# Optimization experiments

Hardware: AMD Instinct MI355X
Metric: run time of the kernel (lower is better)

Reference implementation:

```python
import jax, jax.numpy as jnp
import numpy as np

KERNEL = (7, 7)
NUM_CH = 4
EPS = 1e-06
ROPE_BASE = 10000.0


def _rel_dist():
    coords = [np.arange(k, dtype=np.float32) - k // 2 for k in KERNEL]
    g = np.meshgrid(*coords, indexing='ij')
    d = np.sqrt(sum(gi ** 2 for gi in g))
    return jnp.asarray(d.reshape(-1)), float(d.max())


def silu(x):
    return x * jax.nn.sigmoid(x)


def rmsnorm(x, w):
    rms = jnp.sqrt(jnp.mean(x * x, axis=-1, keepdims=True) + EPS)
    return x / rms * w


def apply_rope(x):
    # x: (B, L, H, D); positions run over dim -2 (matches torch default)
    H, D = x.shape[-2], x.shape[-1]
    half = D // 2
    pos = jnp.arange(H, dtype=jnp.float32)
    freqs = 1.0 / (ROPE_BASE ** (jnp.arange(half, dtype=x.dtype) / half))
    ang = pos[:, None] * freqs  # (H, half)
    cos, sin = jnp.cos(ang), jnp.sin(ang)
    x1, x2 = x[..., :half], x[..., half:2 * half]
    return jnp.concatenate([x1 * cos - x2 * sin, x1 * sin + x2 * cos], axis=-1)


def unfold2d(x):
    # x: (B, Hs, Ws, C) -> (B, Hs, Ws, k1*k2, C), row-major kernel order
    B, Hs, Ws, C = x.shape
    k1, k2 = KERNEL
    xp = jnp.pad(x, ((0, 0), ((k1 - 1) // 2, k1 // 2), ((k2 - 1) // 2, k2 // 2), (0, 0)))
    wins = [xp[:, i:i + Hs, j:j + Ws, :] for i in range(k1) for j in range(k2)]
    return jnp.stack(wins, axis=3)


def setup_inputs() -> dict:
    key = jax.random.key(0)
    ks = jax.random.split(key, 8)
    C = 256
    x = jax.random.normal(ks[0], (2, 64, 64, C), dtype=jnp.float32)
    W_qkv = jax.random.normal(ks[1], (C, 3 * C), dtype=jnp.float32) * 0.02
    w_qnorm = jnp.ones((C // NUM_CH,), dtype=jnp.float32)
    w_knorm = jnp.ones((C // NUM_CH,), dtype=jnp.float32)
    W_wp = jax.random.normal(ks[2], (C, 2 * NUM_CH), dtype=jnp.float32) * 0.02
    b_wp = jax.random.normal(ks[3], (2 * NUM_CH,), dtype=jnp.float32) * 0.02
    w_onorm = jnp.ones((C,), dtype=jnp.float32)
    W_out = jax.random.normal(ks[4], (C, C), dtype=jnp.float32) * 0.02
    W_gate = jax.random.normal(ks[5], (C, C), dtype=jnp.float32) * 0.02
    b_gate = 2.0 * jnp.ones((C,), dtype=jnp.float32)
    return {"x": x, "W_qkv": W_qkv, "w_qnorm": w_qnorm, "w_knorm": w_knorm,
            "W_wp": W_wp, "b_wp": b_wp, "w_onorm": w_onorm, "W_out": W_out,
            "W_gate": W_gate, "b_gate": b_gate}


def reference(x, W_qkv, w_qnorm, w_knorm, W_wp, b_wp, w_onorm, W_out, W_gate, b_gate):
    rel_dist, max_dist = _rel_dist()
    B, Hs, Ws, C = x.shape
    L = Hs * Ws
    H = NUM_CH
    D = C // H
    Wsz = KERNEL[0] * KERNEL[1]
    scale = D ** (-0.5)

    qkv = silu(x @ W_qkv)
    q, k, v = jnp.split(qkv, 3, axis=-1)

    q_flat = apply_rope(rmsnorm(q.reshape(B, L, H, D), w_qnorm))
    k_flat = apply_rope(rmsnorm(k.reshape(B, L, H, D), w_knorm))
    k = k_flat.reshape(B, Hs, Ws, C)

    wp = silu(x @ W_wp + b_wp)  # (B, Hs, Ws, 2H)
    width_raw, sharp_raw = jnp.split(wp, 2, axis=-1)
    width = jax.nn.sigmoid(width_raw) * max_dist + 0.5
    sharpness = jax.nn.sigmoid(sharp_raw) * 9.5 + 0.5

    k_win = unfold2d(k).reshape(B, L, Wsz, H, D)
    v_win = unfold2d(v).reshape(B, L, Wsz, H, D)

    scores = jnp.einsum('blhd,blwhd->blhw', q_flat, k_win) * scale
    width_f = width.reshape(B, L, H, 1)
    sharp_f = sharpness.reshape(B, L, H, 1)
    soft_mask = jax.nn.sigmoid((width_f - rel_dist) * sharp_f)
    scores = scores - (1.0 - soft_mask) * 10000.0
    attn = jax.nn.softmax(scores, axis=-1)

    out = jnp.einsum('blhw,blwhd->blhd', attn, v_win).reshape(B, Hs, Ws, C)
    out = rmsnorm(out, w_onorm)

    gate = jax.nn.sigmoid(silu(v @ W_gate + b_gate))
    merged = gate * v + (1.0 - gate) * out
    return silu(merged @ W_out)
```

## Files before the change

kernel.cpp:

```cpp
#include <hip/hip_runtime.h>
#include <hip/hip_fp16.h>
#include <math.h>

__device__ __forceinline__ float sigm(float x)  { return 1.0f / (1.0f + __expf(-x)); }
__device__ __forceinline__ float siluf(float x) { return x * sigm(x); }

typedef _Float16 half8  __attribute__((ext_vector_type(8)));
typedef _Float16 half4  __attribute__((ext_vector_type(4)));
typedef float    f32x4  __attribute__((ext_vector_type(4)));

__device__ __forceinline__ void gld16(const void* g, void* l) {
    __builtin_amdgcn_global_load_lds(
        (const __attribute__((address_space(1))) unsigned*)g,
        (__attribute__((address_space(3))) unsigned*)l, 16, 0, 0);
}

template <int N>
__device__ __forceinline__ void wait_vmcnt() {
    if constexpr (N == 0)      asm volatile("s_waitcnt vmcnt(0)" ::: "memory");
    else if constexpr (N == 3) asm volatile("s_waitcnt vmcnt(3)" ::: "memory");
    else if constexpr (N == 5) asm volatile("s_waitcnt vmcnt(5)" ::: "memory");
    else if constexpr (N == 6) asm volatile("s_waitcnt vmcnt(6)" ::: "memory");
}

template <int MI, int AMODE>
__device__ __forceinline__ void gemm_core16(
    const __half* __restrict__ A16,
    const __half* __restrict__ Bhi, const __half* __restrict__ Blo,
    int nbs, int m0, int n0, int t, f32x4 (&acc)[MI][4])
{
    __shared__ short As[2][MI * 1024], BsHi[2][4096], BsLo[2][4096];
    const int lane = t & 63, wave = t >> 6;
    const int wm = (wave >> 1) * (MI << 4), wn = (wave & 1) << 6;
    const int fr = lane & 15, fq = lane >> 4;
    constexpr int NL = MI / 2 + 4;

    auto stage = [&](int kb, int buf) {
#pragma unroll
        for (int hf = 0; hf < MI / 2; ++hf) {
            const int rr = wave * (MI << 3) + (hf << 4);
            size_t ga;
            if (AMODE == 0)
                ga = (((size_t)(kb * 8192 + m0 + rr)) << 5) + (lane << 3);
            else
                ga = (((size_t)(m0 + rr + (lane >> 2))) << 8) + (kb << 5) + ((lane & 3) << 3);
            gld16(A16 + ga, &As[buf][rr << 5]);
        }
#pragma unroll
        for (int hf = 0; hf < 2; ++hf) {
            const int rr = (wave << 5) + (hf << 4);
            const size_t gb = (((size_t)(kb * nbs + n0 + rr)) << 5) + (lane << 3);
            gld16(Bhi + gb, &BsHi[buf][rr << 5]);
            gld16(Blo + gb, &BsLo[buf][rr << 5]);
        }
    };

    stage(0, 0);
#pragma unroll
    for (int kb = 0; kb < 8; ++kb) {
        const int cur = kb & 1;
        if (kb < 7) {
            stage(kb + 1, cur ^ 1);
            wait_vmcnt<NL>();
        } else {
            wait_vmcnt<0>();
        }
        __builtin_amdgcn_s_barrier();

        half8 a[MI], bh[4], bl[4];
#pragma unroll
        for (int i = 0; i < MI; ++i)
            a[i] = *(const half8*)&As[cur][((wm + (i << 4) + fr) << 5) + (fq << 3)];
#pragma unroll
        for (int i = 0; i < 4; ++i) {
            const int boff = ((wn + (i << 4) + fr) << 5) + (fq << 3);
            bh[i] = *(const half8*)&BsHi[cur][boff];
            bl[i] = *(const half8*)&BsLo[cur][boff];
        }
#pragma unroll
        for (int mi = 0; mi < MI; ++mi)
#pragma unroll
            for (int ni = 0; ni < 4; ++ni) {
                acc[mi][ni] = __builtin_amdgcn_mfma_f32_16x16x32_f16(a[mi], bh[ni], acc[mi][ni], 0, 0, 0);
                acc[mi][ni] = __builtin_amdgcn_mfma_f32_16x16x32_f16(a[mi], bl[ni], acc[mi][ni], 0, 0, 0);
            }

        if (kb < 7) __builtin_amdgcn_s_barrier();
    }
}

__device__ __forceinline__ void gemm_core64(
    const __half* __restrict__ A16,
    const __half* __restrict__ Bhi, const __half* __restrict__ Blo,
    int m0, int n0, int t, f32x4 (&acc)[4])
{
    __shared__ short As[2][2048], BsHi[2][2048], BsLo[2][2048];
    const int lane = t & 63, wave = t >> 6;
    const int wm = wave << 4;
    const int fr = lane & 15, fq = lane >> 4;

    auto stage = [&](int kb, int buf) {
        const int rr = wave << 4;
        const size_t ga = (((size_t)(m0 + rr + (lane >> 2))) << 8) + (kb << 5) + ((lane & 3) << 3);
        gld16(A16 + ga, &As[buf][rr << 5]);
        const size_t gb = (((size_t)(kb * 256 + n0 + rr)) << 5) + (lane << 3);
        gld16(Bhi + gb, &BsHi[buf][rr << 5]);
        gld16(Blo + gb, &BsLo[buf][rr << 5]);
    };

    stage(0, 0);
#pragma unroll
    for (int kb = 0; kb < 8; ++kb) {
        const int cur = kb & 1;
        if (kb < 7) {
            stage(kb + 1, cur ^ 1);
            wait_vmcnt<3>();
        } else {
            wait_vmcnt<0>();
        }
        __builtin_amdgcn_s_barrier();

        half8 a = *(const half8*)&As[cur][((wm + fr) << 5) + (fq << 3)];
        half8 bh[4], bl[4];
#pragma unroll
        for (int ni = 0; ni < 4; ++ni) {
            const int boff = (((ni << 4) + fr) << 5) + (fq << 3);
            bh[ni] = *(const half8*)&BsHi[cur][boff];
            bl[ni] = *(const half8*)&BsLo[cur][boff];
        }
#pragma unroll
        for (int ni = 0; ni < 4; ++ni) {
            acc[ni] = __builtin_amdgcn_mfma_f32_16x16x32_f16(a, bh[ni], acc[ni], 0, 0, 0);
            acc[ni] = __builtin_amdgcn_mfma_f32_16x16x32_f16(a, bl[ni], acc[ni], 0, 0, 0);
        }

        if (kb < 7) __builtin_amdgcn_s_barrier();
    }
}

__global__ __launch_bounds__(256) void prep_kernel(
    const float* __restrict__ x, const float* __restrict__ Wqkv,
    const float* __restrict__ Wgate, const float* __restrict__ Wout,
    const float* __restrict__ Wwp, const float* __restrict__ bwp,
    __half* __restrict__ xh,
    __half* __restrict__ wqh, __half* __restrict__ wql,
    __half* __restrict__ wgh, __half* __restrict__ wgl,
    __half* __restrict__ woh, __half* __restrict__ wol,
    float* __restrict__ width, float* __restrict__ sharp)
{
    __shared__ float xs[32][260];
    const int t = threadIdx.x;
    const int blk = blockIdx.x;
    if (blk < 256) {
        const int row0 = blk << 5;
        for (int e = t; e < 2048; e += 256) {
            int r = e >> 6, cc = (e & 63) << 2;
            *(float4*)&xs[r][cc] = *(const float4*)&x[(size_t)(row0 + r) * 256 + cc];
        }
        __syncthreads();
        const int r = t >> 3, kb = t & 7;
        __half hibuf[32];
#pragma unroll
        for (int i = 0; i < 32; ++i)
            hibuf[i] = __float2half(xs[r][(kb << 5) + i]);
        const size_t ob = ((size_t)(kb * 8192 + row0 + r)) << 5;
#pragma unroll
        for (int i = 0; i < 4; ++i)
            *(int4*)&xh[ob + (i << 3)] = *(int4*)&hibuf[i << 3];
        float a0 = 0.f, a1 = 0.f, a2 = 0.f, a3 = 0.f;
#pragma unroll 4
        for (int k = 0; k < 256; k += 4) {
            a0 += xs[r][k + 0] * Wwp[(k + 0) * 8 + kb];
            a1 += xs[r][k + 1] * Wwp[(k + 1) * 8 + kb];
            a2 += xs[r][k + 2] * Wwp[(k + 2) * 8 + kb];
            a3 += xs[r][k + 3] * Wwp[(k + 3) * 8 + kb];
        }
        const float acc = (a0 + a1) + (a2 + a3);
        float s = sigm(siluf(acc + bwp[kb]));
        const int row = row0 + r;
        if (kb < 4) width[row * 4 + kb] = s * 4.242640687119285f + 0.5f;
        else        sharp[row * 4 + kb - 4] = s * 9.5f + 0.5f;
    } else {
        const float* W; __half *Whi, *Wlo; int N, nb0, ncnt;
        if (blk < 288)      { W = Wqkv;  Whi = wqh; Wlo = wql; N = 768; nb0 = (blk - 256) * 24; ncnt = 24; }
        else if (blk < 296) { W = Wgate; Whi = wgh; Wlo = wgl; N = 256; nb0 = (blk - 288) * 32; ncnt = 32; }
        else                { W = Wout;  Whi = woh; Wlo = wol; N = 256; nb0 = (blk - 296) * 32; ncnt = 32; }
        for (int j = 0; j < ncnt; ++j)
            xs[j][t] = W[(size_t)t * N + nb0 + j];
        __syncthreads();
        for (int c = t; c < ncnt * 8; c += 256) {
            const int j = c >> 3, kb = c & 7;
            __half hibuf[32], lobuf[32];
#pragma unroll
            for (int i = 0; i < 32; ++i) {
                float v = xs[j][(kb << 5) + i];
                __half hv = __float2half(v);
                hibuf[i] = hv;
                lobuf[i] = __float2half(v - __half2float(hv));
            }
            const size_t ob = ((size_t)(kb * N + nb0 + j)) << 5;
#pragma unroll
            for (int i = 0; i < 4; ++i) {
                *(int4*)&Whi[ob + (i << 3)] = *(int4*)&hibuf[i << 3];
                *(int4*)&Wlo[ob + (i << 3)] = *(int4*)&lobuf[i << 3];
            }
        }
    }
}

__global__ __launch_bounds__(256, 3) void gemm_qkv(
    const __half* __restrict__ xh,
    const __half* __restrict__ wqh, const __half* __restrict__ wql,
    const float* __restrict__ wq, const float* __restrict__ wk,
    __half* __restrict__ qh, __half* __restrict__ kh, __half* __restrict__ vh)
{
    const int t  = threadIdx.x;
    const int m0 = blockIdx.y << 6, n0 = blockIdx.x << 7;
    f32x4 acc[2][4] = {};
    gemm_core16<2, 0>(xh, wqh, wql, 768, m0, n0, t, acc);

    const int lane = t & 63, wave = t >> 6;
    const int wm = (wave >> 1) << 5, wn = (wave & 1) << 6;
    const int fr = lane & 15, fq = lane >> 4;
    const int gc0 = n0 + wn;
    const int seg = gc0 >> 8;
    const int h   = (gc0 >> 6) & 3;
    const int hc0 = h << 6;

#pragma unroll
    for (int mi = 0; mi < 2; ++mi)
#pragma unroll
        for (int ni = 0; ni < 4; ++ni)
#pragma unroll
            for (int r = 0; r < 4; ++r)
                acc[mi][ni][r] = siluf(acc[mi][ni][r]);

    if (seg == 2) {
#pragma unroll
        for (int mi = 0; mi < 2; ++mi)
#pragma unroll
            for (int r = 0; r < 4; ++r) {
                const size_t row = m0 + wm + (mi << 4) + (fq << 2) + r;
#pragma unroll
                for (int ni = 0; ni < 4; ++ni)
                    vh[row * 256 + hc0 + (ni << 4) + fr] = __float2half(acc[mi][ni][r]);
            }
    } else {
        const float* wnorm = seg ? wk : wq;
        float wv[4];
#pragma unroll
        for (int ni = 0; ni < 4; ++ni) wv[ni] = wnorm[(ni << 4) + fr];
        float cs[2], sn[2];
#pragma unroll
        for (int j = 0; j < 2; ++j) {
            const int d = (j << 4) + fr;
            const float freq = powf(10000.f, -(float)d * (1.f / 32.f));
            const float ang = (float)h * freq;
            cs[j] = cosf(ang); sn[j] = sinf(ang);
        }
        __half* dstbase = (seg ? kh : qh);
#pragma unroll
        for (int mi = 0; mi < 2; ++mi)
#pragma unroll
            for (int r = 0; r < 4; ++r) {
                float ss = acc[mi][0][r] * acc[mi][0][r] + acc[mi][1][r] * acc[mi][1][r]
                         + acc[mi][2][r] * acc[mi][2][r] + acc[mi][3][r] * acc[mi][3][r];
                ss += __shfl_xor(ss, 1); ss += __shfl_xor(ss, 2);
                ss += __shfl_xor(ss, 4); ss += __shfl_xor(ss, 8);
                const float rinv = 1.f / sqrtf(ss * (1.f / 64.f) + 1e-6f);
                float xv[4];
#pragma unroll
                for (int ni = 0; ni < 4; ++ni) xv[ni] = acc[mi][ni][r] * rinv * wv[ni];
                const float o0 = xv[0] * cs[0] - xv[2] * sn[0];
                const float o2 = xv[0] * sn[0] + xv[2] * cs[0];
                const float o1 = xv[1] * cs[1] - xv[3] * sn[1];
                const float o3 = xv[1] * sn[1] + xv[3] * cs[1];
                const size_t row = m0 + wm + (mi << 4) + (fq << 2) + r;
                __half* dst = dstbase + row * 256 + hc0;
                dst[fr]      = __float2half(o0);
                dst[16 + fr] = __float2half(o1);
                dst[32 + fr] = __float2half(o2);
                dst[48 + fr] = __float2half(o3);
            }
    }
}

__global__ __launch_bounds__(256, 2) void gemm_gate(
    const __half* __restrict__ vh,
    const __half* __restrict__ wgh, const __half* __restrict__ wgl,
    const float* __restrict__ bias, const float* __restrict__ attn_o,
    const float* __restrict__ sumsq4, const float* __restrict__ w_onorm,
    __half* __restrict__ mh)
{
    const int t  = threadIdx.x;
    const int m0 = blockIdx.y << 6, n0 = blockIdx.x << 6;
    f32x4 acc[4] = {};
    gemm_core64(vh, wgh, wgl, m0, n0, t, acc);

    const int lane = t & 63, wave = t >> 6;
    const int wm = wave << 4;
    const int fr = lane & 15, fq = lane >> 4;

    float rmsf[4];
#pragma unroll
    for (int r = 0; r < 4; ++r) {
        const int m = m0 + wm + (fq << 2) + r;
        float4 s4 = *(const float4*)&sumsq4[(size_t)m * 4];
        rmsf[r] = 1.f / sqrtf((s4.x + s4.y + s4.z + s4.w) * (1.f / 256.f) + 1e-6f);
    }

#pragma unroll
    for (int ni = 0; ni < 4; ++ni) {
        const int n  = n0 + (ni << 4) + fr;
        const int mb = m0 + wm + (fq << 2);
        const float bb  = bias[n];
        const float won = w_onorm[n];
#pragma unroll
        for (int r = 0; r < 4; ++r) {
            const int m = mb + r;
            const float g  = sigm(siluf(acc[ni][r] + bb));
            const float vv = __half2float(vh[(size_t)m * 256 + n]);
            const float oo = attn_o[(size_t)m * 256 + n] * rmsf[r] * won;
            mh[(size_t)m * 256 + n] = __float2half(g * vv + (1.f - g) * oo);
        }
    }
}

__global__ __launch_bounds__(256, 2) void gemm_out(
    const __half* __restrict__ mh,
    const __half* __restrict__ woh, const __half* __restrict__ wol,
    float* __restrict__ out)
{
    const int t  = threadIdx.x;
    const int m0 = blockIdx.y << 6, n0 = blockIdx.x << 6;
    f32x4 acc[4] = {};
    gemm_core64(mh, woh, wol, m0, n0, t, acc);

    const int lane = t & 63, wave = t >> 6;
    const int wm = wave << 4;
    const int fr = lane & 15, fq = lane >> 4;
#pragma unroll
    for (int ni = 0; ni < 4; ++ni) {
        const int n  = n0 + (ni << 4) + fr;
        const int mb = m0 + wm + (fq << 2);
#pragma unroll
        for (int r = 0; r < 4; ++r)
            out[(size_t)(mb + r) * 256 + n] = siluf(acc[ni][r]);
    }
}

#define PT 216

__global__ __launch_bounds__(256, 2) void attn_mfma(
    const __half* __restrict__ qh, const __half* __restrict__ kh,
    const __half* __restrict__ vh, const float* __restrict__ width,
    const float* __restrict__ sharp, float* __restrict__ attn_o,
    float* __restrict__ sumsq4)
{
    __shared__ short smem[27648];
    short* Ksh = smem;
    short* Psh = smem;
    short* Vt  = smem + 13824;

    const int t = threadIdx.x;
    const int lane = t & 63, wave = t >> 6;
    const int fr = lane & 15, fq = lane >> 4;
    const int patch = blockIdx.x, h = blockIdx.y, b = blockIdx.z;
    const int pr0 = (patch >> 3) << 3, pc0 = (patch & 7) << 3;
    const int t0 = (wave * 28) >> 4;

    float wd[4], sh[4]; int lq[4];
#pragma unroll
    for (int r = 0; r < 4; ++r) {
        const int q = (wave << 4) + (fq << 2) + r;
        lq[r] = (pr0 + (q >> 3)) * 64 + pc0 + (q & 7);
        wd[r] = width[((b << 12) + lq[r]) * 4 + h];
        sh[r] = sharp[((b << 12) + lq[r]) * 4 + h];
    }

    const int qrow = (wave << 4) + fr;
    const int lqr = (pr0 + (qrow >> 3)) * 64 + pc0 + (qrow & 7);
    const __half* qptr = qh + (((size_t)(b << 12) + lqr) << 8) + (h << 6) + (fq << 3);
    half8 a0 = *(const half8*)qptr;
    half8 a1 = *(const half8*)(qptr + 32);

    const int srow = t >> 5;
    const int d2 = (t & 31) << 1;
    const size_t cbase = (((size_t)b << 12) * 256) + (size_t)h * 64 + d2;

    unsigned kb[25], vb[25];
#pragma unroll
    for (int p5 = 0; p5 < 25; ++p5) {
        const int prow = p5 * 8 + srow;
        const int pi = prow / 14, pj = prow - pi * 14;
        const int gr = pr0 - 3 + pi, gc = pc0 - 3 + pj;
        const bool ok = (prow < 196) & ((unsigned)gr < 64u) & ((unsigned)gc < 64u);
        const int grc = min(max(gr, 0), 63), gcc = min(max(gc, 0), 63);
        const size_t off = cbase + (size_t)(grc * 64 + gcc) * 256;
        unsigned kv = *(const unsigned*)(kh + off);
        unsigned vv = *(const unsigned*)(vh + off);
        kb[p5] = ok ? kv : 0u;
        vb[p5] = ok ? vv : 0u;
    }

    const int chunk = d2 >> 3, dlo = d2 & 7;
#pragma unroll
    for (int p5 = 0; p5 < 25; ++p5) {
        const int prow = p5 * 8 + srow;
        *(unsigned*)&Ksh[(prow << 6) + ((chunk ^ (prow & 7)) << 3) + dlo] = kb[p5];
        Vt[(d2)     * PT + prow] = (short)(vb[p5] & 0xffffu);
        Vt[(d2 + 1) * PT + prow] = (short)(vb[p5] >> 16);
    }
    if (t < 128) {
        const int rr = 200 + (t >> 4);
        *(unsigned*)&Ksh[(rr << 6) + (((t & 15) ^ ((rr & 7) << 1)) << 2)] = 0u;
    }
    for (int i = t; i < 64 * 20; i += 256)
        Vt[(i / 20) * PT + 196 + (i % 20)] = 0;
    __syncthreads();

    f32x4 sc[8];
#pragma unroll
    for (int tl = 0; tl < 8; ++tl) {
        const int kr = ((t0 + tl) << 4) + fr;
        half8 b0 = *(const half8*)&Ksh[(kr << 6) + (((0 + fq) ^ (kr & 7)) << 3)];
        half8 b1 = *(const half8*)&Ksh[(kr << 6) + (((4 + fq) ^ (kr & 7)) << 3)];
        f32x4 z = {0.f, 0.f, 0.f, 0.f};
        z = __builtin_amdgcn_mfma_f32_16x16x32_f16(a0, b0, z, 0, 0, 0);
        sc[tl] = __builtin_amdgcn_mfma_f32_16x16x32_f16(a1, b1, z, 0, 0, 0);
    }

    float mx[4] = {-3e38f, -3e38f, -3e38f, -3e38f};
#pragma unroll
    for (int tl = 0; tl < 8; ++tl) {
        const int p = ((t0 + tl) << 4) + fr;
        const int pi = p / 14, pj = p - pi * 14;
        const bool pvld = p < 196;
#pragma unroll
        for (int r = 0; r < 4; ++r) {
            const int q = (wave << 4) + (fq << 2) + r;
            const int di = pi - 3 - ((q >> 3) & 7), dj = pj - 3 - (q & 7);
            const bool win = pvld & ((unsigned)(di + 3) <= 6u) & ((unsigned)(dj + 3) <= 6u);
            const float rel = sqrtf((float)(di * di + dj * dj));
            const float mk = sigm((wd[r] - rel) * sh[r]);
            float s = sc[tl][r] * 0.125f - (1.f - mk) * 10000.f;
            s = win ? s : -3e38f;
            sc[tl][r] = s;
            mx[r] = fmaxf(mx[r], s);
        }
    }
#pragma unroll
    for (int r = 0; r < 4; ++r) {
        mx[r] = fmaxf(mx[r], __shfl_xor(mx[r], 1));
        mx[r] = fmaxf(mx[r], __shfl_xor(mx[r], 2));
        mx[r] = fmaxf(mx[r], __shfl_xor(mx[r], 4));
        mx[r] = fmaxf(mx[r], __shfl_xor(mx[r], 8));
    }
    float sm[4] = {0.f, 0.f, 0.f, 0.f};
#pragma unroll
    for (int tl = 0; tl < 8; ++tl)
#pragma unroll
        for (int r = 0; r < 4; ++r) {
            const float e = __expf(sc[tl][r] - mx[r]);
            sc[tl][r] = e; sm[r] += e;
        }
#pragma unroll
    for (int r = 0; r < 4; ++r) {
        sm[r] += __shfl_xor(sm[r], 1);
        sm[r] += __shfl_xor(sm[r], 2);
        sm[r] += __shfl_xor(sm[r], 4);
        sm[r] += __shfl_xor(sm[r], 8);
        sm[r] = 1.f / sm[r];
    }

    __syncthreads();
#pragma unroll
    for (int tl = 0; tl < 8; ++tl)
#pragma unroll
        for (int r = 0; r < 4; ++r) {
            __half pv = __float2half(sc[tl][r] * sm[r]);
            Psh[((wave << 4) + (fq << 2) + r) * PT + ((t0 + tl) << 4) + fr] = *(short*)&pv;
        }
    __syncthreads();

    f32x4 o[4] = {};
    const int pra = (wave << 4) + fr;
    const int cb = t0 << 4;
#pragma unroll
    for (int s = 0; s < 4; ++s) {
        half8 pa = *(const half8*)&Psh[pra * PT + cb + (fq << 3) + (s << 5)];
#pragma unroll
        for (int dt = 0; dt < 4; ++dt) {
            half8 vbf = *(const half8*)&Vt[((dt << 4) + fr) * PT + cb + (fq << 3) + (s << 5)];
            o[dt] = __builtin_amdgcn_mfma_f32_16x16x32_f16(pa, vbf, o[dt], 0, 0, 0);
        }
    }

#pragma unroll
    for (int r = 0; r < 4; ++r) {
        float ss = o[0][r]*o[0][r] + o[1][r]*o[1][r] + o[2][r]*o[2][r] + o[3][r]*o[3][r];
        ss += __shfl_xor(ss, 1); ss += __shfl_xor(ss, 2);
        ss += __shfl_xor(ss, 4); ss += __shfl_xor(ss, 8);
        const size_t rowb = (((size_t)(b << 12) + lq[r]) << 8) + h * 64;
#pragma unroll
        for (int dt = 0; dt < 4; ++dt)
            attn_o[rowb + (dt << 4) + fr] = o[dt][r];
        if (fr == 0) sumsq4[(((b << 12) + lq[r]) << 2) + h] = ss;
    }
}

extern "C" void kernel_launch(void* const* d_in, const int* in_sizes, int n_in,
                              void* d_out, int out_size, void* d_ws, size_t ws_size,
                              hipStream_t stream)
{
    const float* x      = (const float*)d_in[0];
    const float* W_qkv  = (const float*)d_in[1];
    const float* w_qn   = (const float*)d_in[2];
    const float* w_kn   = (const float*)d_in[3];
    const float* W_wp   = (const float*)d_in[4];
    const float* b_wp   = (const float*)d_in[5];
    const float* w_on   = (const float*)d_in[6];
    const float* W_out  = (const float*)d_in[7];
    const float* W_gate = (const float*)d_in[8];
    const float* b_gate = (const float*)d_in[9];
    float* out = (float*)d_out;

    __half* ws16 = (__half*)d_ws;
    __half* xh  = ws16;
    __half* wqh = xh  + 2097152;
    __half* wql = wqh + 196608;
    __half* wgh = wql + 196608;
    __half* wgl = wgh + 65536;
    __half* woh = wgl + 65536;
    __half* wol = woh + 65536;
    __half* qhp = wol + 65536;
    __half* khp = qhp + 2097152;
    __half* vhp = khp + 2097152;
    __half* mh  = vhp + 2097152;
    float* attn_o = (float*)(mh + 2097152);
    float* widthp = attn_o + 2097152;
    float* sharpp = widthp + 32768;
    float* sumsq4 = sharpp + 32768;

    prep_kernel<<<304, 256, 0, stream>>>(x, W_qkv, W_gate, W_out, W_wp, b_wp,
                                         xh, wqh, wql, wgh, wgl, woh, wol,
                                         widthp, sharpp);
    gemm_qkv<<<dim3(6, 128), 256, 0, stream>>>(xh, wqh, wql, w_qn, w_kn,
                                               qhp, khp, vhp);
    attn_mfma<<<dim3(64, 4, 2), 256, 0, stream>>>(qhp, khp, vhp, widthp, sharpp,
                                                  attn_o, sumsq4);
    gemm_gate<<<dim3(4, 128), 256, 0, stream>>>(vhp, wgh, wgl, b_gate,
                                                attn_o, sumsq4, w_on, mh);
    gemm_out<<<dim3(4, 128), 256, 0, stream>>>(mh, woh, wol, out);
}
```

Before: 135.7 us.

## Replace LDS-staged GEMM cores with direct global-to-register double buffering

```diff
diff --git a/kernel.cpp b/kernel.cpp
--- a/kernel.cpp
+++ b/kernel.cpp
@@ -9,132 +9,99 @@
 typedef _Float16 half4  __attribute__((ext_vector_type(4)));
 typedef float    f32x4  __attribute__((ext_vector_type(4)));
 
-__device__ __forceinline__ void gld16(const void* g, void* l) {
-    __builtin_amdgcn_global_load_lds(
-        (const __attribute__((address_space(1))) unsigned*)g,
-        (__attribute__((address_space(3))) unsigned*)l, 16, 0, 0);
-}
-
-template <int N>
-__device__ __forceinline__ void wait_vmcnt() {
-    if constexpr (N == 0)      asm volatile("s_waitcnt vmcnt(0)" ::: "memory");
-    else if constexpr (N == 3) asm volatile("s_waitcnt vmcnt(3)" ::: "memory");
-    else if constexpr (N == 5) asm volatile("s_waitcnt vmcnt(5)" ::: "memory");
-    else if constexpr (N == 6) asm volatile("s_waitcnt vmcnt(6)" ::: "memory");
-}
-
-template <int MI, int AMODE>
-__device__ __forceinline__ void gemm_core16(
+
+template <int AMODE>
+__device__ __forceinline__ void gemm_reg16(
     const __half* __restrict__ A16,
     const __half* __restrict__ Bhi, const __half* __restrict__ Blo,
-    int nbs, int m0, int n0, int t, f32x4 (&acc)[MI][4])
-{
-    __shared__ short As[2][MI * 1024], BsHi[2][4096], BsLo[2][4096];
+    int nbs, int m0, int n0, int t, f32x4 (&acc)[2][4])
+{
     const int lane = t & 63, wave = t >> 6;
-    const int wm = (wave >> 1) * (MI << 4), wn = (wave & 1) << 6;
+    const int wm = (wave >> 1) << 5, wn = (wave & 1) << 6;
     const int fr = lane & 15, fq = lane >> 4;
-    constexpr int NL = MI / 2 + 4;
-
-    auto stage = [&](int kb, int buf) {
-#pragma unroll
-        for (int hf = 0; hf < MI / 2; ++hf) {
-            const int rr = wave * (MI << 3) + (hf << 4);
-            size_t ga;
-            if (AMODE == 0)
-                ga = (((size_t)(kb * 8192 + m0 + rr)) << 5) + (lane << 3);
-            else
-                ga = (((size_t)(m0 + rr + (lane >> 2))) << 8) + (kb << 5) + ((lane & 3) << 3);
-            gld16(A16 + ga, &As[buf][rr << 5]);
-        }
-#pragma unroll
-        for (int hf = 0; hf < 2; ++hf) {
-            const int rr = (wave << 5) + (hf << 4);
-            const size_t gb = (((size_t)(kb * nbs + n0 + rr)) << 5) + (lane << 3);
-            gld16(Bhi + gb, &BsHi[buf][rr << 5]);
-            gld16(Blo + gb, &BsLo[buf][rr << 5]);
-        }
+
+    half8 a[2][2], bh[2][4], bl[2][4];
+
+    auto loadA = [&](int kb, int i) -> half8 {
+        size_t off;
+        if (AMODE == 0)
+            off = (((size_t)(kb * 8192 + m0 + wm + (i << 4) + fr)) << 5) + (fq << 3);
+        else
+            off = (((size_t)(m0 + wm + (i << 4) + fr)) << 8) + (kb << 5) + (fq << 3);
+        return *(const half8*)(A16 + off);
     };
-
-    stage(0, 0);
+    auto loadB = [&](const __half* __restrict__ W, int kb, int ni) -> half8 {
+        const size_t off = (((size_t)(kb * nbs + n0 + wn + (ni << 4) + fr)) << 5) + (fq << 3);
+        return *(const half8*)(W + off);
+    };
+
+#pragma unroll
+    for (int i = 0; i < 2; ++i) a[0][i] = loadA(0, i);
+#pragma unroll
+    for (int ni = 0; ni < 4; ++ni) { bh[0][ni] = loadB(Bhi, 0, ni); bl[0][ni] = loadB(Blo, 0, ni); }
+
 #pragma unroll
     for (int kb = 0; kb < 8; ++kb) {
-        const int cur = kb & 1;
+        const int cur = kb & 1, nxt = cur ^ 1;
         if (kb < 7) {
-            stage(kb + 1, cur ^ 1);
-            wait_vmcnt<NL>();
-        } else {
-            wait_vmcnt<0>();
-        }
-        __builtin_amdgcn_s_barrier();
-
-        half8 a[MI], bh[4], bl[4];
-#pragma unroll
-        for (int i = 0; i < MI; ++i)
-            a[i] = *(const half8*)&As[cur][((wm + (i << 4) + fr) << 5) + (fq << 3)];
-#pragma unroll
-        for (int i = 0; i < 4; ++i) {
-            const int boff = ((wn + (i << 4) + fr) << 5) + (fq << 3);
-            bh[i] = *(const half8*)&BsHi[cur][boff];
-            bl[i] = *(const half8*)&BsLo[cur][boff];
-        }
-#pragma unroll
-        for (int mi = 0; mi < MI; ++mi)
+#pragma unroll
+            for (int i = 0; i < 2; ++i) a[nxt][i] = loadA(kb + 1, i);
 #pragma unroll
             for (int ni = 0; ni < 4; ++ni) {
-                acc[mi][ni] = __builtin_amdgcn_mfma_f32_16x16x32_f16(a[mi], bh[ni], acc[mi][ni], 0, 0, 0);
-                acc[mi][ni] = __builtin_amdgcn_mfma_f32_16x16x32_f16(a[mi], bl[ni], acc[mi][ni], 0, 0, 0);
-            }
-
-        if (kb < 7) __builtin_amdgcn_s_barrier();
-    }
-}
-
-__device__ __forceinline__ void gemm_core64(
+                bh[nxt][ni] = loadB(Bhi, kb + 1, ni);
+                bl[nxt][ni] = loadB(Blo, kb + 1, ni);
+            }
+        }
+#pragma unroll
+        for (int mi = 0; mi < 2; ++mi)
+#pragma unroll
+            for (int ni = 0; ni < 4; ++ni) {
+                acc[mi][ni] = __builtin_amdgcn_mfma_f32_16x16x32_f16(a[cur][mi], bh[cur][ni], acc[mi][ni], 0, 0, 0);
+                acc[mi][ni] = __builtin_amdgcn_mfma_f32_16x16x32_f16(a[cur][mi], bl[cur][ni], acc[mi][ni], 0, 0, 0);
+            }
+    }
+}
+
+__device__ __forceinline__ void gemm_reg64(
     const __half* __restrict__ A16,
     const __half* __restrict__ Bhi, const __half* __restrict__ Blo,
     int m0, int n0, int t, f32x4 (&acc)[4])
 {
-    __shared__ short As[2][2048], BsHi[2][2048], BsLo[2][2048];
     const int lane = t & 63, wave = t >> 6;
     const int wm = wave << 4;
     const int fr = lane & 15, fq = lane >> 4;
 
-    auto stage = [&](int kb, int buf) {
-        const int rr = wave << 4;
-        const size_t ga = (((size_t)(m0 + rr + (lane >> 2))) << 8) + (kb << 5) + ((lane & 3) << 3);
-        gld16(A16 + ga, &As[buf][rr << 5]);
-        const size_t gb = (((size_t)(kb * 256 + n0 + rr)) << 5) + (lane << 3);
-        gld16(Bhi + gb, &BsHi[buf][rr << 5]);
-        gld16(Blo + gb, &BsLo[buf][rr << 5]);
+    half8 a[2], bh[2][4], bl[2][4];
+
+    auto loadA = [&](int kb) -> half8 {
+        const size_t off = (((size_t)(m0 + wm + fr)) << 8) + (kb << 5) + (fq << 3);
+        return *(const half8*)(A16 + off);
     };
-
-    stage(0, 0);
+    auto loadB = [&](const __half* __restrict__ W, int kb, int ni) -> half8 {
+        const size_t off = (((size_t)(kb * 256 + n0 + (ni << 4) + fr)) << 5) + (fq << 3);
+        return *(const half8*)(W + off);
+    };
+
+    a[0] = loadA(0);
+#pragma unroll
+    for (int ni = 0; ni < 4; ++ni) { bh[0][ni] = loadB(Bhi, 0, ni); bl[0][ni] = loadB(Blo, 0, ni); }
+
 #pragma unroll
     for (int kb = 0; kb < 8; ++kb) {
-        const int cur = kb & 1;
+        const int cur = kb & 1, nxt = cur ^ 1;
         if (kb < 7) {
-            stage(kb + 1, cur ^ 1);
-            wait_vmcnt<3>();
-        } else {
-            wait_vmcnt<0>();
-        }
-        __builtin_amdgcn_s_barrier();
-
-        half8 a = *(const half8*)&As[cur][((wm + fr) << 5) + (fq << 3)];
-        half8 bh[4], bl[4];
+            a[nxt] = loadA(kb + 1);
+#pragma unroll
+            for (int ni = 0; ni < 4; ++ni) {
+                bh[nxt][ni] = loadB(Bhi, kb + 1, ni);
+                bl[nxt][ni] = loadB(Blo, kb + 1, ni);
+            }
+        }
 #pragma unroll
         for (int ni = 0; ni < 4; ++ni) {
-            const int boff = (((ni << 4) + fr) << 5) + (fq << 3);
-            bh[ni] = *(const half8*)&BsHi[cur][boff];
-            bl[ni] = *(const half8*)&BsLo[cur][boff];
-        }
-#pragma unroll
-        for (int ni = 0; ni < 4; ++ni) {
-            acc[ni] = __builtin_amdgcn_mfma_f32_16x16x32_f16(a, bh[ni], acc[ni], 0, 0, 0);
-            acc[ni] = __builtin_amdgcn_mfma_f32_16x16x32_f16(a, bl[ni], acc[ni], 0, 0, 0);
-        }
-
-        if (kb < 7) __builtin_amdgcn_s_barrier();
+            acc[ni] = __builtin_amdgcn_mfma_f32_16x16x32_f16(a[cur], bh[cur][ni], acc[ni], 0, 0, 0);
+            acc[ni] = __builtin_amdgcn_mfma_f32_16x16x32_f16(a[cur], bl[cur][ni], acc[ni], 0, 0, 0);
+        }
     }
 }
 
@@ -217,7 +184,7 @@
     const int t  = threadIdx.x;
     const int m0 = blockIdx.y << 6, n0 = blockIdx.x << 7;
     f32x4 acc[2][4] = {};
-    gemm_core16<2, 0>(xh, wqh, wql, 768, m0, n0, t, acc);
+    gemm_reg16<0>(xh, wqh, wql, 768, m0, n0, t, acc);
 
     const int lane = t & 63, wave = t >> 6;
     const int wm = (wave >> 1) << 5, wn = (wave & 1) << 6;
@@ -295,7 +262,7 @@
     const int t  = threadIdx.x;
     const int m0 = blockIdx.y << 6, n0 = blockIdx.x << 6;
     f32x4 acc[4] = {};
-    gemm_core64(vh, wgh, wgl, m0, n0, t, acc);
+    gemm_reg64(vh, wgh, wgl, m0, n0, t, acc);
 
     const int lane = t & 63, wave = t >> 6;
     const int wm = wave << 4;
@@ -334,7 +301,7 @@
     const int t  = threadIdx.x;
     const int m0 = blockIdx.y << 6, n0 = blockIdx.x << 6;
     f32x4 acc[4] = {};
-    gemm_core64(mh, woh, wol, m0, n0, t, acc);
+    gemm_reg64(mh, woh, wol, m0, n0, t, acc);
 
     const int lane = t & 63, wave = t >> 6;
     const int wm = wave << 4;
```

Result: slower. 149.0 us (+9.8%).
